# Optimization experiments

Hardware: AMD Instinct MI355X
Metric: run time of the kernel (lower is better)

Reference implementation:

```python
import jax, jax.numpy as jnp
import numpy as np

N_TOKENS = 4096
BATCH = 32


def setup_inputs() -> dict:
    key = jax.random.key(0)
    ks = jax.random.split(key, 9)
    n = N_TOKENS
    s = 0.02  # small init scale so exp(q*k) stays stable
    inp = {
        "x": jax.random.normal(ks[0], (BATCH, n), dtype=jnp.float32),
        "Wq": s * jax.random.normal(ks[1], (n, n), dtype=jnp.float32),
        "bq": jnp.zeros((n,), dtype=jnp.float32),
        "Wk": s * jax.random.normal(ks[2], (n, n), dtype=jnp.float32),
        "bk": jnp.zeros((n,), dtype=jnp.float32),
        "Wv": s * jax.random.normal(ks[3], (n, n), dtype=jnp.float32),
        "bv": jnp.zeros((n,), dtype=jnp.float32),
        "Wp": s * jax.random.normal(ks[4], (n, n), dtype=jnp.float32),
        "bp": jnp.zeros((n,), dtype=jnp.float32),
    }
    return inp


def reference(x, Wq, bq, Wk, bk, Wv, bv, Wp, bp):
    # Linear layers (torch convention: y = x @ W.T + b)
    q = x @ Wq.T + bq  # [b, n]
    k = x @ Wk.T + bk  # [b, n]
    v = x @ Wv.T + bv  # [b, n]
    # Rank-1 attention: scores[b,i,j] = q_i * k_j, softmax over j
    scores = q[:, :, None] * k[:, None, :]  # [b, n, n]
    w = jax.nn.softmax(scores, axis=2)
    attended = jnp.einsum('bij,bj->bi', w, v)  # [b, n]
    h = jax.nn.silu(x + attended)
    out = jax.nn.silu(h + h @ Wp.T + bp)
    return out
```

## Files before the change

kernel.cpp:

```cpp
#include <hip/hip_runtime.h>
#include <math.h>

#define N 4096
#define BATCH 32

#define NB 64
#define NP 9
#define QLO (-10.0f)
#define QBW 0.3125f
#define QINVBW 3.2f
#define NMOM (NB * 2 * NP)
#define NCHUNK 8

typedef short bf16x8 __attribute__((ext_vector_type(8)));
typedef float f32x4  __attribute__((ext_vector_type(4)));

static __device__ __forceinline__ float fast_exp2(float x) {
#if __has_builtin(__builtin_amdgcn_exp2f)
  return __builtin_amdgcn_exp2f(x);
#else
  return exp2f(x);
#endif
}

static __device__ __forceinline__ unsigned short f2bf_rne(float f) {
  unsigned int u = __float_as_uint(f);
  return (unsigned short)((u + 0x7FFFu + ((u >> 16) & 1u)) >> 16);
}
static __device__ __forceinline__ float bf2f(unsigned short h) {
  return __uint_as_float((unsigned int)h << 16);
}

__device__ const float c_invfact[NP] = {
  1.f, 1.f, 0.5f, 1.f/6.f, 1.f/24.f, 1.f/120.f, 1.f/720.f, 1.f/5040.f, 1.f/40320.f};

__global__ __launch_bounds__(256)
void prep_frags(const float* __restrict__ src, short* __restrict__ dst)
{
  int id = blockIdx.x * 256 + threadIdx.x;
  int narr = id >> 13;
  int rem  = id & 8191;
  int T = rem >> 6;
  int l = rem & 63;
  int b = (l & 15) | ((narr & 1) << 4);
  int k = T * 32 + ((l >> 4) << 3);
  const float* s = &src[(size_t)b * N + k];
  bf16x8 o;
  #pragma unroll
  for (int j = 0; j < 8; ++j) {
    float f = s[j];
    unsigned short h = f2bf_rne(f);
    if (narr >> 1) h = f2bf_rne(f - bf2f(h));
    o[j] = (short)h;
  }
  *(bf16x8*)&dst[(size_t)id * 8] = o;
}

template <int NSTEP, bool PARTIAL, bool SILU>
__device__ __forceinline__ void gemm_mfma_body(
    const float* __restrict__ W, const short* __restrict__ Xf,
    const float* __restrict__ bias, const float* __restrict__ resid,
    float* __restrict__ Y, int kbeg)
{
  const int t = threadIdx.x;
  const int w = t >> 6, l = t & 63;
  const int i0 = blockIdx.x * 16;

  const float* wrow = &W[(size_t)(i0 + (l & 15)) * N + kbeg + w * (NSTEP * 32) + ((l >> 4) << 3)];
  const short* bbase = Xf + (size_t)((kbeg >> 5) + w * NSTEP) * 512 + l * 8;

  f32x4 acc0 = {0.f, 0.f, 0.f, 0.f};
  f32x4 acc1 = {0.f, 0.f, 0.f, 0.f};

  auto cvt = [&](const float4& a, const float4& b, bf16x8& ah, bf16x8& al) {
    #pragma unroll
    for (int e = 0; e < 8; ++e) {
      float x = (e < 4) ? ((const float*)&a)[e] : ((const float*)&b)[e - 4];
      unsigned int u = __float_as_uint(x);
      ah[e] = (short)(u >> 16);
      float r = x - __uint_as_float(u & 0xFFFF0000u);
      al[e] = (short)(__float_as_uint(r) >> 16);
    }
  };

  auto dostep = [&](const float4& wa, const float4& wb, const short* bptr) {
    bf16x8 bh0 = *(const bf16x8*)(bptr);
    bf16x8 bh1 = *(const bf16x8*)(bptr + 65536);
    bf16x8 bl0 = *(const bf16x8*)(bptr + 131072);
    bf16x8 bl1 = *(const bf16x8*)(bptr + 196608);
    bf16x8 ah, al;
    cvt(wa, wb, ah, al);
    acc0 = __builtin_amdgcn_mfma_f32_16x16x32_bf16(ah, bh0, acc0, 0, 0, 0);
    acc1 = __builtin_amdgcn_mfma_f32_16x16x32_bf16(ah, bh1, acc1, 0, 0, 0);
    acc0 = __builtin_amdgcn_mfma_f32_16x16x32_bf16(ah, bl0, acc0, 0, 0, 0);
    acc1 = __builtin_amdgcn_mfma_f32_16x16x32_bf16(ah, bl1, acc1, 0, 0, 0);
    acc0 = __builtin_amdgcn_mfma_f32_16x16x32_bf16(al, bh0, acc0, 0, 0, 0);
    acc1 = __builtin_amdgcn_mfma_f32_16x16x32_bf16(al, bh1, acc1, 0, 0, 0);
  };

  constexpr int NGRP = NSTEP / 4;
  float4 wc[8], wn[8];
  #pragma unroll
  for (int u = 0; u < 4; ++u) {
    wc[2 * u]     = *(const float4*)(wrow + u * 32);
    wc[2 * u + 1] = *(const float4*)(wrow + u * 32 + 4);
  }
  #pragma unroll 1
  for (int g = 0; g < NGRP - 1; ++g) {
    const float* wg = wrow + (g + 1) * 128;
    #pragma unroll
    for (int u = 0; u < 4; ++u) {
      wn[2 * u]     = *(const float4*)(wg + u * 32);
      wn[2 * u + 1] = *(const float4*)(wg + u * 32 + 4);
    }
    const short* bg = bbase + (size_t)g * 2048;
    #pragma unroll
    for (int u = 0; u < 4; ++u) dostep(wc[2 * u], wc[2 * u + 1], bg + u * 512);
    #pragma unroll
    for (int u = 0; u < 8; ++u) wc[u] = wn[u];
  }
  {
    const short* bg = bbase + (size_t)(NGRP - 1) * 2048;
    #pragma unroll
    for (int u = 0; u < 4; ++u) dostep(wc[2 * u], wc[2 * u + 1], bg + u * 512);
  }

  __shared__ float red[4][2][4][64];
  #pragma unroll
  for (int r = 0; r < 4; ++r) { red[w][0][r][l] = acc0[r]; red[w][1][r][l] = acc1[r]; }
  __syncthreads();

  #pragma unroll
  for (int e = t; e < 512; e += 256) {
    int b  = e >> 4;
    int il = e & 15;
    int n  = b >> 4;
    int lw = (b & 15) | ((il >> 2) << 4);
    int r  = il & 3;
    float v = ((red[0][n][r][lw] + red[1][n][r][lw]) +
               (red[2][n][r][lw] + red[3][n][r][lw]));
    int i = i0 + il;
    float y = PARTIAL ? v : (v + bias[i]);
    if (SILU) {
      float z = resid[(size_t)b * N + i] + y;
      y = z / (1.f + fast_exp2(-1.44269504f * z));
    }
    Y[(size_t)b * N + i] = y;
  }
}

__global__ __launch_bounds__(256) __attribute__((amdgpu_waves_per_eu(4)))
void gemm3(const short* __restrict__ Xf,
           const float* __restrict__ W0, const float* __restrict__ b0, float* __restrict__ Y0,
           const float* __restrict__ W1, const float* __restrict__ b1, float* __restrict__ Y1,
           const float* __restrict__ W2, const float* __restrict__ b2, float* __restrict__ Y2)
{
  const float* W = W0; const float* bias = b0; float* Y = Y0;
  if (blockIdx.y == 1) { W = W1; bias = b1; Y = Y1; }
  else if (blockIdx.y == 2) { W = W2; bias = b2; Y = Y2; }
  gemm_mfma_body<32, false, false>(W, Xf, bias, nullptr, Y, 0);
}

__global__ __launch_bounds__(256) __attribute__((amdgpu_waves_per_eu(4)))
void gemm_p(const short* __restrict__ Hf, const float* __restrict__ W,
            float* __restrict__ T0, float* __restrict__ T1,
            float* __restrict__ T2, float* __restrict__ T3)
{
  float* T = T0;
  if (blockIdx.y == 1) T = T1;
  else if (blockIdx.y == 2) T = T2;
  else if (blockIdx.y == 3) T = T3;
  gemm_mfma_body<8, true, false>(W, Hf, nullptr, nullptr, T, blockIdx.y * 1024);
}

__global__ __launch_bounds__(1024, 2)
void moments_a(const float* __restrict__ kk, const float* __restrict__ vv,
               float* __restrict__ P)
{
  const int b = blockIdx.x, chunk = blockIdx.y;
  const int t = threadIdx.x;
  const int wv = t >> 6, m = t & 63;
  const float gam = QLO + ((float)m + 0.5f) * QBW;
  const float gl2e = gam * 1.44269504f;
  float S[NP], T[NP];
  #pragma unroll
  for (int p = 0; p < NP; ++p) { S[p] = 0.f; T[p] = 0.f; }
  const float* kb = &kk[(size_t)b * N + chunk * 512 + wv * 32];
  const float* vb = &vv[(size_t)b * N + chunk * 512 + wv * 32];
  #pragma unroll 4
  for (int jj = 0; jj < 32; ++jj) {
    float kj = kb[jj];
    float vj = vb[jj];
    float e = fast_exp2(gl2e * kj);
    float tp = e;
    S[0] += tp; T[0] = fmaf(tp, vj, T[0]);
    #pragma unroll
    for (int p = 1; p < NP; ++p) { tp *= kj; S[p] += tp; T[p] = fmaf(tp, vj, T[p]); }
  }
  __shared__ float red[16][NMOM];
  #pragma unroll
  for (int p = 0; p < NP; ++p) {
    red[wv][m * 18 + p] = S[p];
    red[wv][m * 18 + NP + p] = T[p];
  }
  __syncthreads();
  for (int e = t; e < NMOM; e += 1024) {
    float s = 0.f;
    #pragma unroll
    for (int w2 = 0; w2 < 16; ++w2) s += red[w2][e];
    P[((size_t)b * NCHUNK + chunk) * NMOM + e] = s;
  }
}

__global__ __launch_bounds__(256)
void moments_b(const float* __restrict__ P, float* __restrict__ M)
{
  int b = blockIdx.x;
  int e = blockIdx.y * 256 + threadIdx.x;
  if (e >= NMOM) return;
  float s = 0.f;
  #pragma unroll
  for (int c = 0; c < NCHUNK; ++c) s += P[((size_t)b * NCHUNK + c) * NMOM + e];
  int p = e % (2 * NP); if (p >= NP) p -= NP;
  M[(size_t)b * NMOM + e] = s * c_invfact[p];
}

__global__ __launch_bounds__(256)
void attn_eval(const float* __restrict__ q, const float* __restrict__ M,
               const float* __restrict__ x, float* __restrict__ h,
               short* __restrict__ Hf)
{
  const int b = blockIdx.x;
  const int i = blockIdx.y * 256 + threadIdx.x;
  __shared__ float cm[NMOM];
  for (int e = threadIdx.x; e < NMOM; e += 256) cm[e] = M[(size_t)b * NMOM + e];
  __syncthreads();
  float qv = q[(size_t)b * N + i];
  float qc = fminf(fmaxf(qv, QLO + 0.01f), -QLO - 0.01f);
  int m = (int)((qc - QLO) * QINVBW);
  float gam = QLO + ((float)m + 0.5f) * QBW;
  float d = qv - gam;
  const float* Sp = &cm[m * 18];
  float f = Sp[NP - 1], g = Sp[2 * NP - 1];
  #pragma unroll
  for (int p = NP - 2; p >= 0; --p) {
    f = fmaf(f, d, Sp[p]);
    g = fmaf(g, d, Sp[NP + p]);
  }
  float att = g / f;
  float z = x[(size_t)b * N + i] + att;
  float hv = z / (1.f + fast_exp2(-1.44269504f * z));
  h[(size_t)b * N + i] = hv;
  unsigned short hi = f2bf_rne(hv);
  unsigned short lo = f2bf_rne(hv - bf2f(hi));
  size_t base = (size_t)(b >> 4) * 65536 + (size_t)(i >> 5) * 512
              + (size_t)((b & 15) | (((i >> 3) & 3) << 4)) * 8 + (size_t)(i & 7);
  Hf[base] = (short)hi;
  Hf[base + 131072] = (short)lo;
}

__global__ __launch_bounds__(256)
void finalize_kernel(const float* __restrict__ h, const float* __restrict__ T0,
                     const float* __restrict__ T1, const float* __restrict__ T2,
                     const float* __restrict__ T3, const float* __restrict__ bp,
                     float* __restrict__ out)
{
  int idx = (blockIdx.x * 256 + threadIdx.x) * 4;
  int i = idx & (N - 1);
  float4 hv = *(const float4*)&h[idx];
  float4 a  = *(const float4*)&T0[idx];
  float4 b  = *(const float4*)&T1[idx];
  float4 c  = *(const float4*)&T2[idx];
  float4 dd = *(const float4*)&T3[idx];
  float4 bb = *(const float4*)&bp[i];
  float4 z, o;
  z.x = hv.x + (a.x + b.x) + (c.x + dd.x) + bb.x;
  z.y = hv.y + (a.y + b.y) + (c.y + dd.y) + bb.y;
  z.z = hv.z + (a.z + b.z) + (c.z + dd.z) + bb.z;
  z.w = hv.w + (a.w + b.w) + (c.w + dd.w) + bb.w;
  o.x = z.x / (1.f + fast_exp2(-1.44269504f * z.x));
  o.y = z.y / (1.f + fast_exp2(-1.44269504f * z.y));
  o.z = z.z / (1.f + fast_exp2(-1.44269504f * z.z));
  o.w = z.w / (1.f + fast_exp2(-1.44269504f * z.w));
  *(float4*)&out[idx] = o;
}

extern "C" void kernel_launch(void* const* d_in, const int* in_sizes, int n_in,
                              void* d_out, int out_size, void* d_ws, size_t ws_size,
                              hipStream_t stream)
{
  const float* x  = (const float*)d_in[0];
  const float* Wq = (const float*)d_in[1];
  const float* bq = (const float*)d_in[2];
  const float* Wk = (const float*)d_in[3];
  const float* bk = (const float*)d_in[4];
  const float* Wv = (const float*)d_in[5];
  const float* bv = (const float*)d_in[6];
  const float* Wp = (const float*)d_in[7];
  const float* bp = (const float*)d_in[8];
  float* out = (float*)d_out;

  float* q  = (float*)d_ws;
  float* kk = q  + BATCH * N;
  float* vv = kk + BATCH * N;
  float* h  = vv + BATCH * N;
  float* T3 = h  + BATCH * N;
  short* Xf = (short*)(T3 + BATCH * N);
  short* Hf = Xf + 262144;
  float* P  = (float*)(Hf + 262144);
  float* M  = P + (size_t)BATCH * NCHUNK * NMOM;

  prep_frags<<<dim3(128), 256, 0, stream>>>(x, Xf);
  gemm3<<<dim3(256, 3), 256, 0, stream>>>(Xf, Wq, bq, q, Wk, bk, kk, Wv, bv, vv);
  moments_a<<<dim3(BATCH, NCHUNK), 1024, 0, stream>>>(kk, vv, P);
  moments_b<<<dim3(BATCH, 5), 256, 0, stream>>>(P, M);
  attn_eval<<<dim3(BATCH, 16), 256, 0, stream>>>(q, M, x, h, Hf);
  gemm_p<<<dim3(256, 4), 256, 0, stream>>>(Hf, Wp, q, kk, vv, T3);
  finalize_kernel<<<dim3(128), 256, 0, stream>>>(h, q, kk, vv, T3, bp, out);
}
```

Measured before the change: 297.1 us.

## Stage weight tiles into LDS with async global_load_lds double buffering

Replaces register prefetching of fp32 weight rows in the MFMA GEMM with asynchronous global-to-LDS copies into a per-wave double buffer, synchronised with manual vmcnt waits. The aim is to overlap weight streaming with bf16 split conversion and MFMA work while using fewer VGPRs. It adds an LDS round trip and relies on hand-written waitcnt ordering, which could be fragile. The unused SILU epilogue path is also dropped.

```diff
diff --git a/kernel.cpp b/kernel.cpp
--- a/kernel.cpp
+++ b/kernel.cpp
@@ -33,6 +33,21 @@
 
 __device__ const float c_invfact[NP] = {
   1.f, 1.f, 0.5f, 1.f/6.f, 1.f/24.f, 1.f/120.f, 1.f/720.f, 1.f/5040.f, 1.f/40320.f};
+
+#if __has_builtin(__builtin_amdgcn_global_load_lds)
+#define HAVE_ASYNC_LDS 1
+#else
+#define HAVE_ASYNC_LDS 0
+#endif
+static __device__ __forceinline__ void async_cp16(const float* g, float* lds_base, int lane) {
+#if HAVE_ASYNC_LDS
+  __builtin_amdgcn_global_load_lds(
+      (const __attribute__((address_space(1))) void*)g,
+      (__attribute__((address_space(3))) void*)lds_base, 16, 0, 0);
+#else
+  ((float4*)lds_base)[lane] = *(const float4*)g;
+#endif
+}
 
 __global__ __launch_bounds__(256)
 void prep_frags(const float* __restrict__ src, short* __restrict__ dst)
@@ -56,21 +71,35 @@
   *(bf16x8*)&dst[(size_t)id * 8] = o;
 }
 
-template <int NSTEP, bool PARTIAL, bool SILU>
+template <int NTILE, bool PARTIAL>
 __device__ __forceinline__ void gemm_mfma_body(
     const float* __restrict__ W, const short* __restrict__ Xf,
-    const float* __restrict__ bias, const float* __restrict__ resid,
-    float* __restrict__ Y, int kbeg)
-{
+    const float* __restrict__ bias, float* __restrict__ Y, int kbeg)
+{
+  constexpr int NSTEP = NTILE * 2;
+  __shared__ __align__(16) union GSm {
+    float stg[4][2][1024];
+    float red[4][2][4][64];
+  } sm;
   const int t = threadIdx.x;
   const int w = t >> 6, l = t & 63;
   const int i0 = blockIdx.x * 16;
-
-  const float* wrow = &W[(size_t)(i0 + (l & 15)) * N + kbeg + w * (NSTEP * 32) + ((l >> 4) << 3)];
+  const int rr = l & 15, kg = l >> 4;
+
+  const float* wbase = &W[(size_t)(i0 + rr) * N + kbeg + w * (NTILE * 64) + kg * 8];
   const short* bbase = Xf + (size_t)((kbeg >> 5) + w * NSTEP) * 512 + l * 8;
 
   f32x4 acc0 = {0.f, 0.f, 0.f, 0.f};
   f32x4 acc1 = {0.f, 0.f, 0.f, 0.f};
+
+  auto stage = [&](int buf, int tt) {
+    float* dst = &sm.stg[w][buf][0];
+    const float* g = wbase + tt * 64;
+    async_cp16(g,      dst,       l);
+    async_cp16(g + 4,  dst + 256, l);
+    async_cp16(g + 32, dst + 512, l);
+    async_cp16(g + 36, dst + 768, l);
+  };
 
   auto cvt = [&](const float4& a, const float4& b, bf16x8& ah, bf16x8& al) {
     #pragma unroll
@@ -83,51 +112,57 @@
     }
   };
 
-  auto dostep = [&](const float4& wa, const float4& wb, const short* bptr) {
-    bf16x8 bh0 = *(const bf16x8*)(bptr);
-    bf16x8 bh1 = *(const bf16x8*)(bptr + 65536);
-    bf16x8 bl0 = *(const bf16x8*)(bptr + 131072);
-    bf16x8 bl1 = *(const bf16x8*)(bptr + 196608);
-    bf16x8 ah, al;
-    cvt(wa, wb, ah, al);
-    acc0 = __builtin_amdgcn_mfma_f32_16x16x32_bf16(ah, bh0, acc0, 0, 0, 0);
-    acc1 = __builtin_amdgcn_mfma_f32_16x16x32_bf16(ah, bh1, acc1, 0, 0, 0);
-    acc0 = __builtin_amdgcn_mfma_f32_16x16x32_bf16(ah, bl0, acc0, 0, 0, 0);
-    acc1 = __builtin_amdgcn_mfma_f32_16x16x32_bf16(ah, bl1, acc1, 0, 0, 0);
-    acc0 = __builtin_amdgcn_mfma_f32_16x16x32_bf16(al, bh0, acc0, 0, 0, 0);
-    acc1 = __builtin_amdgcn_mfma_f32_16x16x32_bf16(al, bh1, acc1, 0, 0, 0);
-  };
-
-  constexpr int NGRP = NSTEP / 4;
-  float4 wc[8], wn[8];
-  #pragma unroll
-  for (int u = 0; u < 4; ++u) {
-    wc[2 * u]     = *(const float4*)(wrow + u * 32);
-    wc[2 * u + 1] = *(const float4*)(wrow + u * 32 + 4);
-  }
+  stage(0, 0);
+  int buf = 0;
   #pragma unroll 1
-  for (int g = 0; g < NGRP - 1; ++g) {
-    const float* wg = wrow + (g + 1) * 128;
-    #pragma unroll
-    for (int u = 0; u < 4; ++u) {
-      wn[2 * u]     = *(const float4*)(wg + u * 32);
-      wn[2 * u + 1] = *(const float4*)(wg + u * 32 + 4);
+  for (int tt = 0; tt < NTILE; ++tt) {
+    bf16x8 bf0h0 = *(const bf16x8*)(bbase + (size_t)(tt * 2) * 512);
+    bf16x8 bf0h1 = *(const bf16x8*)(bbase + (size_t)(tt * 2) * 512 + 65536);
+    bf16x8 bf0l0 = *(const bf16x8*)(bbase + (size_t)(tt * 2) * 512 + 131072);
+    bf16x8 bf0l1 = *(const bf16x8*)(bbase + (size_t)(tt * 2) * 512 + 196608);
+    bf16x8 bf1h0 = *(const bf16x8*)(bbase + (size_t)(tt * 2 + 1) * 512);
+    bf16x8 bf1h1 = *(const bf16x8*)(bbase + (size_t)(tt * 2 + 1) * 512 + 65536);
+    bf16x8 bf1l0 = *(const bf16x8*)(bbase + (size_t)(tt * 2 + 1) * 512 + 131072);
+    bf16x8 bf1l1 = *(const bf16x8*)(bbase + (size_t)(tt * 2 + 1) * 512 + 196608);
+    __builtin_amdgcn_sched_barrier(0);
+    if (tt + 1 < NTILE) {
+      stage(buf ^ 1, tt + 1);
+      asm volatile("s_waitcnt vmcnt(4)" ::: "memory");
+    } else {
+      asm volatile("s_waitcnt vmcnt(0)" ::: "memory");
     }
-    const short* bg = bbase + (size_t)g * 2048;
-    #pragma unroll
-    for (int u = 0; u < 4; ++u) dostep(wc[2 * u], wc[2 * u + 1], bg + u * 512);
-    #pragma unroll
-    for (int u = 0; u < 8; ++u) wc[u] = wn[u];
-  }
-  {
-    const short* bg = bbase + (size_t)(NGRP - 1) * 2048;
-    #pragma unroll
-    for (int u = 0; u < 4; ++u) dostep(wc[2 * u], wc[2 * u + 1], bg + u * 512);
-  }
-
-  __shared__ float red[4][2][4][64];
-  #pragma unroll
-  for (int r = 0; r < 4; ++r) { red[w][0][r][l] = acc0[r]; red[w][1][r][l] = acc1[r]; }
+    __builtin_amdgcn_sched_barrier(0);
+
+    {
+      float4 a0 = *(const float4*)&sm.stg[w][buf][0 * 512 + l * 4];
+      float4 a1 = *(const float4*)&sm.stg[w][buf][0 * 512 + 256 + l * 4];
+      bf16x8 ah, al;
+      cvt(a0, a1, ah, al);
+      acc0 = __builtin_amdgcn_mfma_f32_16x16x32_bf16(ah, bf0h0, acc0, 0, 0, 0);
+      acc1 = __builtin_amdgcn_mfma_f32_16x16x32_bf16(ah, bf0h1, acc1, 0, 0, 0);
+      acc0 = __builtin_amdgcn_mfma_f32_16x16x32_bf16(ah, bf0l0, acc0, 0, 0, 0);
+      acc1 = __builtin_amdgcn_mfma_f32_16x16x32_bf16(ah, bf0l1, acc1, 0, 0, 0);
+      acc0 = __builtin_amdgcn_mfma_f32_16x16x32_bf16(al, bf0h0, acc0, 0, 0, 0);
+      acc1 = __builtin_amdgcn_mfma_f32_16x16x32_bf16(al, bf0h1, acc1, 0, 0, 0);
+    }
+    {
+      float4 a0 = *(const float4*)&sm.stg[w][buf][1 * 512 + l * 4];
+      float4 a1 = *(const float4*)&sm.stg[w][buf][1 * 512 + 256 + l * 4];
+      bf16x8 ah, al;
+      cvt(a0, a1, ah, al);
+      acc0 = __builtin_amdgcn_mfma_f32_16x16x32_bf16(ah, bf1h0, acc0, 0, 0, 0);
+      acc1 = __builtin_amdgcn_mfma_f32_16x16x32_bf16(ah, bf1h1, acc1, 0, 0, 0);
+      acc0 = __builtin_amdgcn_mfma_f32_16x16x32_bf16(ah, bf1l0, acc0, 0, 0, 0);
+      acc1 = __builtin_amdgcn_mfma_f32_16x16x32_bf16(ah, bf1l1, acc1, 0, 0, 0);
+      acc0 = __builtin_amdgcn_mfma_f32_16x16x32_bf16(al, bf1h0, acc0, 0, 0, 0);
+      acc1 = __builtin_amdgcn_mfma_f32_16x16x32_bf16(al, bf1h1, acc1, 0, 0, 0);
+    }
+    buf ^= 1;
+  }
+  __syncthreads();
+
+  #pragma unroll
+  for (int r = 0; r < 4; ++r) { sm.red[w][0][r][l] = acc0[r]; sm.red[w][1][r][l] = acc1[r]; }
   __syncthreads();
 
   #pragma unroll
@@ -137,15 +172,10 @@
     int n  = b >> 4;
     int lw = (b & 15) | ((il >> 2) << 4);
     int r  = il & 3;
-    float v = ((red[0][n][r][lw] + red[1][n][r][lw]) +
-               (red[2][n][r][lw] + red[3][n][r][lw]));
+    float v = ((sm.red[0][n][r][lw] + sm.red[1][n][r][lw]) +
+               (sm.red[2][n][r][lw] + sm.red[3][n][r][lw]));
     int i = i0 + il;
-    float y = PARTIAL ? v : (v + bias[i]);
-    if (SILU) {
-      float z = resid[(size_t)b * N + i] + y;
-      y = z / (1.f + fast_exp2(-1.44269504f * z));
-    }
-    Y[(size_t)b * N + i] = y;
+    Y[(size_t)b * N + i] = PARTIAL ? v : (v + bias[i]);
   }
 }
 
@@ -158,7 +188,7 @@
   const float* W = W0; const float* bias = b0; float* Y = Y0;
   if (blockIdx.y == 1) { W = W1; bias = b1; Y = Y1; }
   else if (blockIdx.y == 2) { W = W2; bias = b2; Y = Y2; }
-  gemm_mfma_body<32, false, false>(W, Xf, bias, nullptr, Y, 0);
+  gemm_mfma_body<16, false>(W, Xf, bias, Y, 0);
 }
 
 __global__ __launch_bounds__(256) __attribute__((amdgpu_waves_per_eu(4)))
@@ -170,7 +200,7 @@
   if (blockIdx.y == 1) T = T1;
   else if (blockIdx.y == 2) T = T2;
   else if (blockIdx.y == 3) T = T3;
-  gemm_mfma_body<8, true, false>(W, Hf, nullptr, nullptr, T, blockIdx.y * 1024);
+  gemm_mfma_body<4, true>(W, Hf, nullptr, T, blockIdx.y * 1024);
 }
 
 __global__ __launch_bounds__(1024, 2)
```

After: 293.8 us. About the same (-1.1%).

## Split-K QKV GEMM across 8-wave blocks and fold moment reduction into consumers

Applied to the files above, without the earlier changes.

The QKV GEMM now uses split-K over two halves with 512-thread blocks (8 waves), doubling the grid to 1536 blocks, and writes partial sums to a shared workspace. Bias addition and partial-sum combination move into moments_a (staged through LDS) and attn_eval. The moments_b kernel is removed by merging its reduction into attn_eval, and the explicit register double-buffering of W loads is replaced by a simple unrolled loop. The aim is more parallelism for the weight-streaming GEMMs and one fewer launch. The cost is extra partial-sum traffic and reliance on the compiler for load scheduling.

```diff
diff --git a/kernel.cpp b/kernel.cpp
--- a/kernel.cpp
+++ b/kernel.cpp
@@ -56,10 +56,9 @@
   *(bf16x8*)&dst[(size_t)id * 8] = o;
 }
 
-template <int NSTEP, bool PARTIAL, bool SILU>
+template <int NSTEP, int NWAVES>
 __device__ __forceinline__ void gemm_mfma_body(
     const float* __restrict__ W, const short* __restrict__ Xf,
-    const float* __restrict__ bias, const float* __restrict__ resid,
     float* __restrict__ Y, int kbeg)
 {
   const int t = threadIdx.x;
@@ -72,125 +71,98 @@
   f32x4 acc0 = {0.f, 0.f, 0.f, 0.f};
   f32x4 acc1 = {0.f, 0.f, 0.f, 0.f};
 
-  auto cvt = [&](const float4& a, const float4& b, bf16x8& ah, bf16x8& al) {
+  #pragma unroll 4
+  for (int s = 0; s < NSTEP; ++s) {
+    float4 wa = *(const float4*)(wrow + s * 32);
+    float4 wb = *(const float4*)(wrow + s * 32 + 4);
+    bf16x8 bh0 = *(const bf16x8*)(bbase + (size_t)s * 512);
+    bf16x8 bh1 = *(const bf16x8*)(bbase + (size_t)s * 512 + 65536);
+    bf16x8 bl0 = *(const bf16x8*)(bbase + (size_t)s * 512 + 131072);
+    bf16x8 bl1 = *(const bf16x8*)(bbase + (size_t)s * 512 + 196608);
+    bf16x8 ah, al;
     #pragma unroll
     for (int e = 0; e < 8; ++e) {
-      float x = (e < 4) ? ((const float*)&a)[e] : ((const float*)&b)[e - 4];
+      float x = (e < 4) ? ((const float*)&wa)[e] : ((const float*)&wb)[e - 4];
       unsigned int u = __float_as_uint(x);
       ah[e] = (short)(u >> 16);
       float r = x - __uint_as_float(u & 0xFFFF0000u);
       al[e] = (short)(__float_as_uint(r) >> 16);
     }
-  };
-
-  auto dostep = [&](const float4& wa, const float4& wb, const short* bptr) {
-    bf16x8 bh0 = *(const bf16x8*)(bptr);
-    bf16x8 bh1 = *(const bf16x8*)(bptr + 65536);
-    bf16x8 bl0 = *(const bf16x8*)(bptr + 131072);
-    bf16x8 bl1 = *(const bf16x8*)(bptr + 196608);
-    bf16x8 ah, al;
-    cvt(wa, wb, ah, al);
     acc0 = __builtin_amdgcn_mfma_f32_16x16x32_bf16(ah, bh0, acc0, 0, 0, 0);
     acc1 = __builtin_amdgcn_mfma_f32_16x16x32_bf16(ah, bh1, acc1, 0, 0, 0);
     acc0 = __builtin_amdgcn_mfma_f32_16x16x32_bf16(ah, bl0, acc0, 0, 0, 0);
     acc1 = __builtin_amdgcn_mfma_f32_16x16x32_bf16(ah, bl1, acc1, 0, 0, 0);
     acc0 = __builtin_amdgcn_mfma_f32_16x16x32_bf16(al, bh0, acc0, 0, 0, 0);
     acc1 = __builtin_amdgcn_mfma_f32_16x16x32_bf16(al, bh1, acc1, 0, 0, 0);
-  };
-
-  constexpr int NGRP = NSTEP / 4;
-  float4 wc[8], wn[8];
-  #pragma unroll
-  for (int u = 0; u < 4; ++u) {
-    wc[2 * u]     = *(const float4*)(wrow + u * 32);
-    wc[2 * u + 1] = *(const float4*)(wrow + u * 32 + 4);
-  }
-  #pragma unroll 1
-  for (int g = 0; g < NGRP - 1; ++g) {
-    const float* wg = wrow + (g + 1) * 128;
-    #pragma unroll
-    for (int u = 0; u < 4; ++u) {
-      wn[2 * u]     = *(const float4*)(wg + u * 32);
-      wn[2 * u + 1] = *(const float4*)(wg + u * 32 + 4);
-    }
-    const short* bg = bbase + (size_t)g * 2048;
-    #pragma unroll
-    for (int u = 0; u < 4; ++u) dostep(wc[2 * u], wc[2 * u + 1], bg + u * 512);
-    #pragma unroll
-    for (int u = 0; u < 8; ++u) wc[u] = wn[u];
-  }
-  {
-    const short* bg = bbase + (size_t)(NGRP - 1) * 2048;
-    #pragma unroll
-    for (int u = 0; u < 4; ++u) dostep(wc[2 * u], wc[2 * u + 1], bg + u * 512);
-  }
-
-  __shared__ float red[4][2][4][64];
+  }
+
+  __shared__ float red[NWAVES][2][4][64];
   #pragma unroll
   for (int r = 0; r < 4; ++r) { red[w][0][r][l] = acc0[r]; red[w][1][r][l] = acc1[r]; }
   __syncthreads();
 
   #pragma unroll
-  for (int e = t; e < 512; e += 256) {
+  for (int e = t; e < 512; e += NWAVES * 64) {
     int b  = e >> 4;
     int il = e & 15;
     int n  = b >> 4;
     int lw = (b & 15) | ((il >> 2) << 4);
     int r  = il & 3;
-    float v = ((red[0][n][r][lw] + red[1][n][r][lw]) +
-               (red[2][n][r][lw] + red[3][n][r][lw]));
-    int i = i0 + il;
-    float y = PARTIAL ? v : (v + bias[i]);
-    if (SILU) {
-      float z = resid[(size_t)b * N + i] + y;
-      y = z / (1.f + fast_exp2(-1.44269504f * z));
-    }
-    Y[(size_t)b * N + i] = y;
-  }
-}
-
-__global__ __launch_bounds__(256) __attribute__((amdgpu_waves_per_eu(4)))
+    float v = 0.f;
+    #pragma unroll
+    for (int w2 = 0; w2 < NWAVES; ++w2) v += red[w2][n][r][lw];
+    Y[(size_t)b * N + i0 + il] = v;
+  }
+}
+
+__global__ __launch_bounds__(512) __attribute__((amdgpu_waves_per_eu(8)))
 void gemm3(const short* __restrict__ Xf,
-           const float* __restrict__ W0, const float* __restrict__ b0, float* __restrict__ Y0,
-           const float* __restrict__ W1, const float* __restrict__ b1, float* __restrict__ Y1,
-           const float* __restrict__ W2, const float* __restrict__ b2, float* __restrict__ Y2)
-{
-  const float* W = W0; const float* bias = b0; float* Y = Y0;
-  if (blockIdx.y == 1) { W = W1; bias = b1; Y = Y1; }
-  else if (blockIdx.y == 2) { W = W2; bias = b2; Y = Y2; }
-  gemm_mfma_body<32, false, false>(W, Xf, bias, nullptr, Y, 0);
-}
-
-__global__ __launch_bounds__(256) __attribute__((amdgpu_waves_per_eu(4)))
+           const float* __restrict__ W0, const float* __restrict__ W1,
+           const float* __restrict__ W2, float* __restrict__ GP)
+{
+  int m = blockIdx.y >> 1;
+  const float* W = (m == 0) ? W0 : (m == 1) ? W1 : W2;
+  gemm_mfma_body<8, 8>(W, Xf, GP + (size_t)blockIdx.y * (BATCH * N), (blockIdx.y & 1) * 2048);
+}
+
+__global__ __launch_bounds__(512) __attribute__((amdgpu_waves_per_eu(8)))
 void gemm_p(const short* __restrict__ Hf, const float* __restrict__ W,
-            float* __restrict__ T0, float* __restrict__ T1,
-            float* __restrict__ T2, float* __restrict__ T3)
-{
-  float* T = T0;
-  if (blockIdx.y == 1) T = T1;
-  else if (blockIdx.y == 2) T = T2;
-  else if (blockIdx.y == 3) T = T3;
-  gemm_mfma_body<8, true, false>(W, Hf, nullptr, nullptr, T, blockIdx.y * 1024);
+            float* __restrict__ GP)
+{
+  gemm_mfma_body<4, 8>(W, Hf, GP + (size_t)blockIdx.y * (BATCH * N), blockIdx.y * 1024);
 }
 
 __global__ __launch_bounds__(1024, 2)
-void moments_a(const float* __restrict__ kk, const float* __restrict__ vv,
-               float* __restrict__ P)
+void moments_a(const float* __restrict__ GP, const float* __restrict__ bk,
+               const float* __restrict__ bv, float* __restrict__ P)
 {
   const int b = blockIdx.x, chunk = blockIdx.y;
   const int t = threadIdx.x;
   const int wv = t >> 6, m = t & 63;
+
+  __shared__ float ksm[512], vsm[512];
+  {
+    const float* GP2 = GP + (size_t)2 * BATCH * N;
+    const float* GP3 = GP + (size_t)3 * BATCH * N;
+    const float* GP4 = GP + (size_t)4 * BATCH * N;
+    const float* GP5 = GP + (size_t)5 * BATCH * N;
+    int col = chunk * 512 + (t & 511);
+    size_t o = (size_t)b * N + col;
+    if (t < 512) ksm[t] = GP2[o] + GP3[o] + bk[col];
+    else         vsm[t & 511] = GP4[o] + GP5[o] + bv[col];
+  }
+  __syncthreads();
+
   const float gam = QLO + ((float)m + 0.5f) * QBW;
   const float gl2e = gam * 1.44269504f;
   float S[NP], T[NP];
   #pragma unroll
   for (int p = 0; p < NP; ++p) { S[p] = 0.f; T[p] = 0.f; }
-  const float* kb = &kk[(size_t)b * N + chunk * 512 + wv * 32];
-  const float* vb = &vv[(size_t)b * N + chunk * 512 + wv * 32];
+  const int jb = wv * 32;
   #pragma unroll 4
   for (int jj = 0; jj < 32; ++jj) {
-    float kj = kb[jj];
-    float vj = vb[jj];
+    float kj = ksm[jb + jj];
+    float vj = vsm[jb + jj];
     float e = fast_exp2(gl2e * kj);
     float tp = e;
     S[0] += tp; T[0] = fmaf(tp, vj, T[0]);
@@ -213,29 +185,23 @@
 }
 
 __global__ __launch_bounds__(256)
-void moments_b(const float* __restrict__ P, float* __restrict__ M)
-{
-  int b = blockIdx.x;
-  int e = blockIdx.y * 256 + threadIdx.x;
-  if (e >= NMOM) return;
-  float s = 0.f;
-  #pragma unroll
-  for (int c = 0; c < NCHUNK; ++c) s += P[((size_t)b * NCHUNK + c) * NMOM + e];
-  int p = e % (2 * NP); if (p >= NP) p -= NP;
-  M[(size_t)b * NMOM + e] = s * c_invfact[p];
-}
-
-__global__ __launch_bounds__(256)
-void attn_eval(const float* __restrict__ q, const float* __restrict__ M,
-               const float* __restrict__ x, float* __restrict__ h,
-               short* __restrict__ Hf)
+void attn_eval(const float* __restrict__ GP, const float* __restrict__ bq,
+               const float* __restrict__ P, const float* __restrict__ x,
+               float* __restrict__ h, short* __restrict__ Hf)
 {
   const int b = blockIdx.x;
   const int i = blockIdx.y * 256 + threadIdx.x;
   __shared__ float cm[NMOM];
-  for (int e = threadIdx.x; e < NMOM; e += 256) cm[e] = M[(size_t)b * NMOM + e];
-  __syncthreads();
-  float qv = q[(size_t)b * N + i];
+  for (int e = threadIdx.x; e < NMOM; e += 256) {
+    float s = 0.f;
+    #pragma unroll
+    for (int c = 0; c < NCHUNK; ++c) s += P[((size_t)b * NCHUNK + c) * NMOM + e];
+    int p = e % (2 * NP); if (p >= NP) p -= NP;
+    cm[e] = s * c_invfact[p];
+  }
+  __syncthreads();
+  size_t o = (size_t)b * N + i;
+  float qv = GP[o] + GP[(size_t)BATCH * N + o] + bq[i];
   float qc = fminf(fmaxf(qv, QLO + 0.01f), -QLO - 0.01f);
   int m = (int)((qc - QLO) * QINVBW);
   float gam = QLO + ((float)m + 0.5f) * QBW;
@@ -248,9 +214,9 @@
     g = fmaf(g, d, Sp[NP + p]);
   }
   float att = g / f;
-  float z = x[(size_t)b * N + i] + att;
+  float z = x[o] + att;
   float hv = z / (1.f + fast_exp2(-1.44269504f * z));
-  h[(size_t)b * N + i] = hv;
+  h[o] = hv;
   unsigned short hi = f2bf_rne(hv);
   unsigned short lo = f2bf_rne(hv - bf2f(hi));
   size_t base = (size_t)(b >> 4) * 65536 + (size_t)(i >> 5) * 512
@@ -260,24 +226,26 @@
 }
 
 __global__ __launch_bounds__(256)
-void finalize_kernel(const float* __restrict__ h, const float* __restrict__ T0,
-                     const float* __restrict__ T1, const float* __restrict__ T2,
-                     const float* __restrict__ T3, const float* __restrict__ bp,
-                     float* __restrict__ out)
+void finalize_kernel(const float* __restrict__ h, const float* __restrict__ GP,
+                     const float* __restrict__ bp, float* __restrict__ out)
 {
   int idx = (blockIdx.x * 256 + threadIdx.x) * 4;
   int i = idx & (N - 1);
+  const float* T0 = GP;
+  const float* T1 = GP + (size_t)1 * BATCH * N;
+  const float* T2 = GP + (size_t)2 * BATCH * N;
+  const float* T3 = GP + (size_t)3 * BATCH * N;
   float4 hv = *(const float4*)&h[idx];
   float4 a  = *(const float4*)&T0[idx];
-  float4 b  = *(const float4*)&T1[idx];
+  float4 bb2 = *(const float4*)&T1[idx];
   float4 c  = *(const float4*)&T2[idx];
   float4 dd = *(const float4*)&T3[idx];
   float4 bb = *(const float4*)&bp[i];
   float4 z, o;
-  z.x = hv.x + (a.x + b.x) + (c.x + dd.x) + bb.x;
-  z.y = hv.y + (a.y + b.y) + (c.y + dd.y) + bb.y;
-  z.z = hv.z + (a.z + b.z) + (c.z + dd.z) + bb.z;
-  z.w = hv.w + (a.w + b.w) + (c.w + dd.w) + bb.w;
+  z.x = hv.x + (a.x + bb2.x) + (c.x + dd.x) + bb.x;
+  z.y = hv.y + (a.y + bb2.y) + (c.y + dd.y) + bb.y;
+  z.z = hv.z + (a.z + bb2.z) + (c.z + dd.z) + bb.z;
+  z.w = hv.w + (a.w + bb2.w) + (c.w + dd.w) + bb.w;
   o.x = z.x / (1.f + fast_exp2(-1.44269504f * z.x));
   o.y = z.y / (1.f + fast_exp2(-1.44269504f * z.y));
   o.z = z.z / (1.f + fast_exp2(-1.44269504f * z.z));
@@ -300,21 +268,16 @@
   const float* bp = (const float*)d_in[8];
   float* out = (float*)d_out;
 
-  float* q  = (float*)d_ws;
-  float* kk = q  + BATCH * N;
-  float* vv = kk + BATCH * N;
-  float* h  = vv + BATCH * N;
-  float* T3 = h  + BATCH * N;
-  short* Xf = (short*)(T3 + BATCH * N);
+  float* GP = (float*)d_ws;
+  float* h  = GP + (size_t)6 * BATCH * N;
+  short* Xf = (short*)(h + BATCH * N);
   short* Hf = Xf + 262144;
   float* P  = (float*)(Hf + 262144);
-  float* M  = P + (size_t)BATCH * NCHUNK * NMOM;
 
   prep_frags<<<dim3(128), 256, 0, stream>>>(x, Xf);
-  gemm3<<<dim3(256, 3), 256, 0, stream>>>(Xf, Wq, bq, q, Wk, bk, kk, Wv, bv, vv);
-  moments_a<<<dim3(BATCH, NCHUNK), 1024, 0, stream>>>(kk, vv, P);
-  moments_b<<<dim3(BATCH, 5), 256, 0, stream>>>(P, M);
-  attn_eval<<<dim3(BATCH, 16), 256, 0, stream>>>(q, M, x, h, Hf);
-  gemm_p<<<dim3(256, 4), 256, 0, stream>>>(Hf, Wp, q, kk, vv, T3);
-  finalize_kernel<<<dim3(128), 256, 0, stream>>>(h, q, kk, vv, T3, bp, out);
-}
+  gemm3<<<dim3(256, 6), 512, 0, stream>>>(Xf, Wq, Wk, Wv, GP);
+  moments_a<<<dim3(BATCH, NCHUNK), 1024, 0, stream>>>(GP, bk, bv, P);
+  attn_eval<<<dim3(BATCH, 16), 256, 0, stream>>>(GP, bq, P, x, h, Hf);
+  gemm_p<<<dim3(256, 4), 512, 0, stream>>>(Hf, Wp, GP);
+  finalize_kernel<<<dim3(128), 256, 0, stream>>>(h, GP, bp, out);
+}
```

Measured after the change: 285.3 us. 4.0% less time.
